# Kernel tuning notes

Measured on AMD Instinct MI355X. Metric: run time of the kernel, lower is better.

## Reference

```python
import jax, jax.numpy as jnp
import numpy as np
import math

N_HEADS = 16
EMBD = 1024
D_HEAD = EMBD // N_HEADS


def setup_inputs() -> dict:
    key = jax.random.key(0)
    ks = jax.random.split(key, 5)
    s = 1.0 / math.sqrt(EMBD)
    return {
        "x": jax.random.normal(ks[0], (2, 2048, EMBD), dtype=jnp.float32),
        "w_in": jax.random.normal(ks[1], (EMBD, 3 * EMBD), dtype=jnp.float32) * s,
        "b_in": jax.random.normal(ks[2], (3 * EMBD,), dtype=jnp.float32) * 0.02,
        "w_out": jax.random.normal(ks[3], (EMBD, EMBD), dtype=jnp.float32) * s,
        "b_out": jax.random.normal(ks[4], (EMBD,), dtype=jnp.float32) * 0.02,
    }


def reference(x, w_in, b_in, w_out, b_out):
    # x: [B, S, D]
    B, S, D = x.shape
    qkv = x @ w_in + b_in                      # [B, S, 3D]
    q, k, v = jnp.split(qkv, 3, axis=-1)
    # [B, S, H, dh] -> [B, H, S, dh]
    def heads(t):
        return t.reshape(B, S, N_HEADS, D_HEAD).transpose(0, 2, 1, 3)
    q, k, v = heads(q), heads(k), heads(v)
    scores = jnp.einsum("bhqd,bhkd->bhqk", q, k)  # [B, H, S, S]
    # causal mask applied before scaling (as in original; -inf invariant to scale)
    causal = jnp.tril(jnp.ones((S, S), dtype=bool))
    scores = jnp.where(causal, scores, -jnp.inf)
    scores = scores / jnp.asarray(math.sqrt(D_HEAD), dtype=scores.dtype)
    attn = jax.nn.softmax(scores, axis=-1)
    out = jnp.einsum("bhqk,bhkd->bhqd", attn, v)  # [B, H, S, dh]
    out = out.transpose(0, 2, 1, 3).reshape(B, S, D)
    return out @ w_out + b_out
```

## Files before the change

kernel.cpp:

```cpp
#include <hip/hip_runtime.h>
#include <stdint.h>

#define DEVI __device__ __forceinline__

typedef __attribute__((ext_vector_type(8))) short short8;
typedef __attribute__((ext_vector_type(4))) float f32x4;
typedef __attribute__((ext_vector_type(4))) uint32_t u32x4;

DEVI unsigned short f2bf(float f) {
    union { float f; uint32_t u; } v; v.f = f;
    return (unsigned short)((v.u + 0x7FFFu + ((v.u >> 16) & 1u)) >> 16);
}

DEVI uint32_t cvtpk_bf16(float a, float b) {
    uint32_t r;
    asm("v_cvt_pk_bf16_f32 %0, %1, %2" : "=v"(r) : "v"(a), "v"(b));
    return r;
}

DEVI void perm32(uint32_t &a, uint32_t &b) {
    asm("v_permlane32_swap_b32 %0, %1" : "+v"(a), "+v"(b));
}
DEVI void perm16(uint32_t &a, uint32_t &b) {
    asm("v_permlane16_swap_b32 %0, %1" : "+v"(a), "+v"(b));
}

DEVI void gload16(const void* g, void* l) {
    __builtin_amdgcn_global_load_lds(
        (const __attribute__((address_space(1))) unsigned int*)g,
        (__attribute__((address_space(3))) unsigned int*)l, 16, 0, 0);
}

__global__ void k_cvt(const float* __restrict__ in, ushort* __restrict__ out, int n4) {
    int i = blockIdx.x * blockDim.x + threadIdx.x;
    int stride = gridDim.x * blockDim.x;
    for (; i < n4; i += stride) {
        float4 v = ((const float4*)in)[i];
        ushort4 o;
        o.x = f2bf(v.x); o.y = f2bf(v.y); o.z = f2bf(v.z); o.w = f2bf(v.w);
        ((ushort4*)out)[i] = o;
    }
}

__global__ void k_tcvt(const float* __restrict__ in, ushort* __restrict__ out, int R, int C) {
    __shared__ float t[32][33];
    int c0 = blockIdx.x * 32, r0 = blockIdx.y * 32;
    int lr = threadIdx.x >> 5, lc = threadIdx.x & 31;
    #pragma unroll
    for (int i = 0; i < 4; i++)
        t[lr + 8*i][lc] = in[(size_t)(r0 + lr + 8*i)*C + c0 + lc];
    __syncthreads();
    #pragma unroll
    for (int i = 0; i < 4; i++)
        out[(size_t)(c0 + lr + 8*i)*R + r0 + lc] = f2bf(t[lc][lr + 8*i]);
}

template<int MODE, int NJ>
__global__ __launch_bounds__(256, 2) void k_gemm(
    const ushort* __restrict__ A, const ushort* __restrict__ Bt,
    const float* __restrict__ bias,
    ushort* __restrict__ oQ, ushort* __restrict__ oK, ushort* __restrict__ oV,
    float* __restrict__ oF,
    int M, int N, int K, int S)
{
    __shared__ __align__(16) ushort As[128*64];
    __shared__ __align__(16) ushort Bs[NJ*32*64];
    const int tid = threadIdx.x;
    const int w = tid >> 6, l = tid & 63;

    int lin = blockIdx.y * gridDim.x + blockIdx.x;
    int nwg = gridDim.x * gridDim.y;
    int swz = (lin & 7) * (nwg >> 3) + (lin >> 3);
    const int m0 = (swz / gridDim.x) * 128, n0 = (swz % gridDim.x) * (NJ*32);

    const int wr = (w >> 1) * 64, wc = (w & 1) * (NJ*16);
    const int fr = l & 15, fg = l >> 4;
    const int lr8 = l >> 3;
    const int slot = (l & 7) ^ lr8;

    f32x4 acc[4][NJ] = {};

    const ushort* Abase = A + (size_t)(m0 + w*32 + lr8) * K + slot*8;
    const ushort* Bbase = Bt + (size_t)(n0 + w*(NJ*8) + lr8) * K + slot*8;

    for (int k0 = 0; k0 < K; k0 += 64) {
        __syncthreads();
        #pragma unroll
        for (int i = 0; i < 4; i++)
            gload16(Abase + (size_t)(8*i)*K + k0, &As[(w*32 + 8*i)*64]);
        #pragma unroll
        for (int i = 0; i < NJ; i++)
            gload16(Bbase + (size_t)(8*i)*K + k0, &Bs[(w*(NJ*8) + 8*i)*64]);
        __syncthreads();
        #pragma unroll
        for (int kk = 0; kk < 2; kk++) {
            short8 af[4], bfr[NJ];
            #pragma unroll
            for (int i = 0; i < 4; i++) {
                int ra = wr + i*16 + fr;
                af[i] = *(const short8*)((const char*)As + ra*128 + ((kk*64 + fg*16) ^ ((ra & 7) << 4)));
            }
            #pragma unroll
            for (int j = 0; j < NJ; j++) {
                int rb = wc + j*16 + fr;
                bfr[j] = *(const short8*)((const char*)Bs + rb*128 + ((kk*64 + fg*16) ^ ((rb & 7) << 4)));
            }
            #pragma unroll
            for (int i = 0; i < 4; i++)
                #pragma unroll
                for (int j = 0; j < NJ; j++)
                    acc[i][j] = __builtin_amdgcn_mfma_f32_16x16x32_bf16(af[i], bfr[j], acc[i][j], 0, 0, 0);
        }
    }

    if (MODE == 1) {
        #pragma unroll
        for (int j = 0; j < NJ; j++) {
            int n = n0 + wc + j*16 + fr;
            float bv = bias[n];
            #pragma unroll
            for (int i = 0; i < 4; i++) {
                int mrow = m0 + wr + i*16 + fg*4;
                #pragma unroll
                for (int r = 0; r < 4; r++)
                    oF[(size_t)(mrow + r)*N + n] = acc[i][j][r] + bv;
            }
        }
    } else {
        #pragma unroll
        for (int j = 0; j < NJ; j++) {
            int n = n0 + wc + j*16 + fr;
            int region = n >> 10;
            int h = (n & 1023) >> 6;
            int d = n & 63;
            float bv = bias[n];
            float scl = (region == 0) ? 0.18033688011112042f : 1.0f;
            #pragma unroll
            for (int i = 0; i < 4; i++) {
                int mrow = m0 + wr + i*16 + fg*4;
                int b = mrow >> 11;
                int s = mrow & 2047;
                if (region < 2) {
                    ushort* dst = (region == 0 ? oQ : oK) + ((size_t)(b*16 + h)*S)*64 + (size_t)d;
                    #pragma unroll
                    for (int r = 0; r < 4; r++)
                        dst[(size_t)(s + r)*64] = f2bf((acc[i][j][r] + bv) * scl);
                } else {
                    ushort* dst = oV + ((size_t)(b*16 + h)*64 + d)*S + s;
                    ushort4 pk;
                    pk.x = f2bf(acc[i][j][0] + bv);
                    pk.y = f2bf(acc[i][j][1] + bv);
                    pk.z = f2bf(acc[i][j][2] + bv);
                    pk.w = f2bf(acc[i][j][3] + bv);
                    *(ushort4*)dst = pk;
                }
            }
        }
    }
}

__global__ __launch_bounds__(128, 2) void k_attn(
    const ushort* __restrict__ Q,
    const ushort* __restrict__ Kb,
    const ushort* __restrict__ Vt,
    ushort* __restrict__ O,
    int S)
{
    __shared__ __align__(16) ushort Kt[2][64*64];
    __shared__ __align__(16) ushort Vs[2][64*64];

    const int tid = threadIdx.x, w = tid >> 6, l = tid & 63;
    const int bid = blockIdx.x;
    const int half = bid >> 9;
    const int r_ = bid & 511;
    const int h = r_ & 15, b = (r_ >> 4) & 1, p = r_ >> 5;
    const int qt = half ? p : (31 - p);
    const int bh = b * 16 + h;
    const int qw = qt * 64 + w * 32;
    const int fr = l & 15, fg = l >> 4;

    short8 qf[2][2];
    {
        const ushort* qp = Q + ((size_t)bh*S + qw + fr)*64 + fg*8;
        qf[0][0] = *(const short8*)(qp);
        qf[0][1] = *(const short8*)(qp + 32);
        qf[1][0] = *(const short8*)(qp + 16*64);
        qf[1][1] = *(const short8*)(qp + 16*64 + 32);
    }

    float l_[2] = {0.f, 0.f};
    f32x4 o_[2][4] = {};

    const int lr8 = l >> 3;
    const int slot = (l & 7) ^ lr8;
    const ushort* Ksrc = Kb + (size_t)bh*S*64;
    const ushort* Vsrc = Vt + (size_t)bh*64*S;

    const int nt = qt + 1;

    auto stage = [&](int buf, int j0) {
        #pragma unroll
        for (int i = 0; i < 4; i++) {
            int rb = w*32 + i*8;
            gload16(Ksrc + (size_t)(j0 + rb + lr8)*64 + slot*8, &Kt[buf][rb*64]);
            gload16(Vsrc + (size_t)(rb + lr8)*S + j0 + slot*8, &Vs[buf][rb*64]);
        }
    };

    stage(0, 0);
    __syncthreads();
    int cur = 0;

    for (int jt = 0; jt < nt; jt++) {
        const int j0 = jt * 64;
        if (jt + 1 < nt) stage(cur ^ 1, j0 + 64);

        f32x4 sa[2][4] = {};
        __builtin_amdgcn_s_setprio(1);
        #pragma unroll
        for (int kk = 0; kk < 2; kk++) {
            short8 kf[4];
            #pragma unroll
            for (int f = 0; f < 4; f++) {
                int row = f*16 + fr;
                kf[f] = *(const short8*)((const char*)Kt[cur] + row*128 + ((kk*64 + fg*16) ^ ((row & 7) << 4)));
            }
            #pragma unroll
            for (int t = 0; t < 2; t++)
                #pragma unroll
                for (int f = 0; f < 4; f++)
                    sa[t][f] = __builtin_amdgcn_mfma_f32_16x16x32_bf16(kf[f], qf[t][kk], sa[t][f], 0, 0, 0);
        }
        __builtin_amdgcn_s_setprio(0);

        if (jt == nt - 1) {
            #pragma unroll
            for (int t = 0; t < 2; t++) {
                int qg = qw + t*16 + fr;
                #pragma unroll
                for (int f = 0; f < 4; f++) {
                    int base = j0 + f*16 + fg*4 - qg;
                    #pragma unroll
                    for (int r = 0; r < 4; r++)
                        if (base + r > 0) sa[t][f][r] = -1e30f;
                }
            }
        }

        uint32_t cw[2][4][2];
        #pragma unroll
        for (int t = 0; t < 2; t++)
            #pragma unroll
            for (int f = 0; f < 4; f++) {
                float p0 = __builtin_amdgcn_exp2f(sa[t][f][0]);
                float p1 = __builtin_amdgcn_exp2f(sa[t][f][1]);
                float p2 = __builtin_amdgcn_exp2f(sa[t][f][2]);
                float p3 = __builtin_amdgcn_exp2f(sa[t][f][3]);
                l_[t] += (p0 + p1) + (p2 + p3);
                cw[t][f][0] = cvtpk_bf16(p0, p1);
                cw[t][f][1] = cvtpk_bf16(p2, p3);
            }

        __builtin_amdgcn_s_setprio(1);
        #pragma unroll
        for (int kk = 0; kk < 2; kk++) {
            short8 pf[2];
            #pragma unroll
            for (int t = 0; t < 2; t++) {
                uint32_t a0 = cw[t][2*kk][0], b0 = cw[t][2*kk + 1][0];
                perm32(a0, b0); perm16(a0, b0);
                uint32_t a1 = cw[t][2*kk][1], b1 = cw[t][2*kk + 1][1];
                perm32(a1, b1); perm16(a1, b1);
                u32x4 uw; uw[0] = a0; uw[1] = a1; uw[2] = b0; uw[3] = b1;
                pf[t] = __builtin_bit_cast(short8, uw);
            }
            #pragma unroll
            for (int f = 0; f < 4; f++) {
                int row = f*16 + fr;
                short8 vf = *(const short8*)((const char*)Vs[cur] + row*128 + ((kk*64 + fg*16) ^ ((row & 7) << 4)));
                #pragma unroll
                for (int t = 0; t < 2; t++)
                    o_[t][f] = __builtin_amdgcn_mfma_f32_16x16x32_bf16(vf, pf[t], o_[t][f], 0, 0, 0);
            }
        }
        __builtin_amdgcn_s_setprio(0);

        __syncthreads();
        cur ^= 1;
    }

    #pragma unroll
    for (int t = 0; t < 2; t++) {
        l_[t] += __shfl_xor(l_[t], 16);
        l_[t] += __shfl_xor(l_[t], 32);
    }

    #pragma unroll
    for (int t = 0; t < 2; t++) {
        float inv = 1.0f / l_[t];
        int qg = qw + t*16 + fr;
        #pragma unroll
        for (int f = 0; f < 4; f++) {
            ushort4 pk;
            pk.x = f2bf(o_[t][f][0] * inv);
            pk.y = f2bf(o_[t][f][1] * inv);
            pk.z = f2bf(o_[t][f][2] * inv);
            pk.w = f2bf(o_[t][f][3] * inv);
            *(ushort4*)&O[((size_t)(b*S + qg))*1024 + h*64 + f*16 + fg*4] = pk;
        }
    }
}

extern "C" void kernel_launch(void* const* d_in, const int* in_sizes, int n_in,
                              void* d_out, int out_size, void* d_ws, size_t ws_size,
                              hipStream_t stream)
{
    const float* x     = (const float*)d_in[0];
    const float* w_in  = (const float*)d_in[1];
    const float* b_in  = (const float*)d_in[2];
    const float* w_out = (const float*)d_in[3];
    const float* b_out = (const float*)d_in[4];
    float* out = (float*)d_out;

    const int B = 2, S = 2048, D = 1024, H = 16;
    const int M = B * S;

    if (ws_size < (40u << 20)) return;
    char* ws = (char*)d_ws;
    ushort* xb     = (ushort*)(ws);
    ushort* w_inT  = (ushort*)(ws + (8u << 20));
    ushort* w_outT = (ushort*)(ws + (14u << 20));
    ushort* qb     = (ushort*)(ws + (16u << 20));
    ushort* kb     = (ushort*)(ws + (24u << 20));
    ushort* vtb    = (ushort*)(ws + (32u << 20));

    k_cvt<<<2048, 256, 0, stream>>>(x, xb, M*D/4);
    k_tcvt<<<dim3(3*D/32, D/32), 256, 0, stream>>>(w_in, w_inT, D, 3*D);
    k_tcvt<<<dim3(D/32, D/32), 256, 0, stream>>>(w_out, w_outT, D, D);
    k_gemm<0,4><<<dim3(3*D/128, M/128), 256, 0, stream>>>(xb, w_inT, b_in, qb, kb, vtb, nullptr, M, 3*D, D, S);
    k_attn<<<1024, 128, 0, stream>>>(qb, kb, vtb, xb, S);
    k_gemm<1,2><<<dim3(D/64, M/128), 256, 0, stream>>>(xb, w_outT, b_out, nullptr, nullptr, nullptr, out, M, D, D, S);
}
```

Before: 108.0 us.

## Split long causal query tiles across two KV chunks and add combine kernel

The longer query tiles (qt 16-31) are now processed by two blocks, each covering half of the KV range. The shorter tiles stay as single blocks, which raises the attention grid from 1024 to 1536 blocks. Each split block writes its unnormalized bf16 partial output and row sums to workspace, and a new k_comb kernel adds the halves and normalizes them. The goal is to even out the causal workload and shorten the tail of long blocks. In exchange it adds a kernel launch, extra global traffic for the partials, and some bf16 rounding of the unnormalized partial sums.

Measured after the change: 109.5 us. No clear change (+1.4%).

```diff
diff --git a/kernel.cpp b/kernel.cpp
--- a/kernel.cpp
+++ b/kernel.cpp
@@ -10,6 +10,11 @@
 DEVI unsigned short f2bf(float f) {
     union { float f; uint32_t u; } v; v.f = f;
     return (unsigned short)((v.u + 0x7FFFu + ((v.u >> 16) & 1u)) >> 16);
+}
+
+DEVI float bf2f(unsigned short u) {
+    union { uint32_t u; float f; } v; v.u = ((uint32_t)u) << 16;
+    return v.f;
 }
 
 DEVI uint32_t cvtpk_bf16(float a, float b) {
@@ -164,6 +169,8 @@
     const ushort* __restrict__ Kb,
     const ushort* __restrict__ Vt,
     ushort* __restrict__ O,
+    ushort* __restrict__ po,
+    float* __restrict__ pl,
     int S)
 {
     __shared__ __align__(16) ushort Kt[2][64*64];
@@ -171,13 +178,24 @@
 
     const int tid = threadIdx.x, w = tid >> 6, l = tid & 63;
     const int bid = blockIdx.x;
-    const int half = bid >> 9;
-    const int r_ = bid & 511;
-    const int h = r_ & 15, b = (r_ >> 4) & 1, p = r_ >> 5;
-    const int qt = half ? p : (31 - p);
-    const int bh = b * 16 + h;
+    int qt, c, bh;
+    if (bid < 1024) {
+        bh = bid & 31;
+        c = (bid >> 5) & 1;
+        qt = 31 - (bid >> 6);
+    } else {
+        int r = bid - 1024;
+        bh = r & 31;
+        c = -1;
+        qt = 15 - (r >> 5);
+    }
+    const int b = bh >> 4, h = bh & 15;
     const int qw = qt * 64 + w * 32;
     const int fr = l & 15, fg = l >> 4;
+
+    const int len0 = (qt + 2) >> 1;
+    const int t0 = (c == 1) ? len0 : 0;
+    const int t1 = (c == 0) ? len0 : qt + 1;
 
     short8 qf[2][2];
     {
@@ -196,8 +214,6 @@
     const ushort* Ksrc = Kb + (size_t)bh*S*64;
     const ushort* Vsrc = Vt + (size_t)bh*64*S;
 
-    const int nt = qt + 1;
-
     auto stage = [&](int buf, int j0) {
         #pragma unroll
         for (int i = 0; i < 4; i++) {
@@ -207,13 +223,13 @@
         }
     };
 
-    stage(0, 0);
+    stage(0, t0 * 64);
     __syncthreads();
     int cur = 0;
 
-    for (int jt = 0; jt < nt; jt++) {
+    for (int jt = t0; jt < t1; jt++) {
         const int j0 = jt * 64;
-        if (jt + 1 < nt) stage(cur ^ 1, j0 + 64);
+        if (jt + 1 < t1) stage(cur ^ 1, j0 + 64);
 
         f32x4 sa[2][4] = {};
         __builtin_amdgcn_s_setprio(1);
@@ -233,7 +249,7 @@
         }
         __builtin_amdgcn_s_setprio(0);
 
-        if (jt == nt - 1) {
+        if (jt == qt) {
             #pragma unroll
             for (int t = 0; t < 2; t++) {
                 int qg = qw + t*16 + fr;
@@ -295,19 +311,68 @@
         l_[t] += __shfl_xor(l_[t], 32);
     }
 
+    if (c < 0) {
+        #pragma unroll
+        for (int t = 0; t < 2; t++) {
+            float inv = 1.0f / l_[t];
+            int qg = qw + t*16 + fr;
+            #pragma unroll
+            for (int f = 0; f < 4; f++) {
+                ushort4 pk;
+                pk.x = f2bf(o_[t][f][0] * inv);
+                pk.y = f2bf(o_[t][f][1] * inv);
+                pk.z = f2bf(o_[t][f][2] * inv);
+                pk.w = f2bf(o_[t][f][3] * inv);
+                *(ushort4*)&O[((size_t)(b*S + qg))*1024 + h*64 + f*16 + fg*4] = pk;
+            }
+        }
+    } else {
+        const int idx = (((31 - qt) << 1) | c) * 32 + bh;
+        ushort* pob = po + ((size_t)idx * 2 + w) * 2048;
+        #pragma unroll
+        for (int t = 0; t < 2; t++) {
+            #pragma unroll
+            for (int f = 0; f < 4; f++) {
+                uint2 pk;
+                pk.x = cvtpk_bf16(o_[t][f][0], o_[t][f][1]);
+                pk.y = cvtpk_bf16(o_[t][f][2], o_[t][f][3]);
+                *(uint2*)(pob + (t*4 + f)*256 + fr*16 + fg*4) = pk;
+            }
+            if (fg == 0) pl[(size_t)idx*64 + w*32 + t*16 + fr] = l_[t];
+        }
+    }
+}
+
+__global__ __launch_bounds__(256) void k_comb(
+    const ushort* __restrict__ po, const float* __restrict__ pl,
+    ushort* __restrict__ O, int S)
+{
+    const int bx = blockIdx.x;
+    const int qt = 31 - (bx >> 5);
+    const int bh = bx & 31;
+    const int b = bh >> 4, h = bh & 15;
+    const int iA = ((31 - qt) << 1) * 32 + bh;
+    const int iB = iA + 32;
+    const float* la = pl + (size_t)iA * 64;
+    const float* lb = pl + (size_t)iB * 64;
+
     #pragma unroll
-    for (int t = 0; t < 2; t++) {
-        float inv = 1.0f / l_[t];
-        int qg = qw + t*16 + fr;
-        #pragma unroll
-        for (int f = 0; f < 4; f++) {
-            ushort4 pk;
-            pk.x = f2bf(o_[t][f][0] * inv);
-            pk.y = f2bf(o_[t][f][1] * inv);
-            pk.z = f2bf(o_[t][f][2] * inv);
-            pk.w = f2bf(o_[t][f][3] * inv);
-            *(ushort4*)&O[((size_t)(b*S + qg))*1024 + h*64 + f*16 + fg*4] = pk;
-        }
+    for (int k = 0; k < 4; k++) {
+        int ss = threadIdx.x + 256 * k;
+        int w = (ss >> 9) & 1, t = (ss >> 8) & 1, f = (ss >> 6) & 3, fr = (ss >> 2) & 15, fg = ss & 3;
+        int g = ss & 511;
+        int row = w*32 + t*16 + fr;
+        ushort4 va = *(const ushort4*)(po + ((size_t)iA * 2 + w) * 2048 + g * 4);
+        ushort4 vb = *(const ushort4*)(po + ((size_t)iB * 2 + w) * 2048 + g * 4);
+        float den = la[row] + lb[row];
+        float inv = 1.0f / fmaxf(den, 1e-30f);
+        ushort4 pk;
+        pk.x = f2bf((bf2f(va.x) + bf2f(vb.x)) * inv);
+        pk.y = f2bf((bf2f(va.y) + bf2f(vb.y)) * inv);
+        pk.z = f2bf((bf2f(va.z) + bf2f(vb.z)) * inv);
+        pk.w = f2bf((bf2f(va.w) + bf2f(vb.w)) * inv);
+        int q = qt*64 + row;
+        *(ushort4*)&O[((size_t)(b*S + q))*1024 + h*64 + f*16 + fg*4] = pk;
     }
 }
 
@@ -325,7 +390,7 @@
     const int B = 2, S = 2048, D = 1024, H = 16;
     const int M = B * S;
 
-    if (ws_size < (40u << 20)) return;
+    if (ws_size < (52u << 20)) return;
     char* ws = (char*)d_ws;
     ushort* xb     = (ushort*)(ws);
     ushort* w_inT  = (ushort*)(ws + (8u << 20));
@@ -333,11 +398,14 @@
     ushort* qb     = (ushort*)(ws + (16u << 20));
     ushort* kb     = (ushort*)(ws + (24u << 20));
     ushort* vtb    = (ushort*)(ws + (32u << 20));
+    ushort* po     = (ushort*)(ws + (40u << 20));
+    float*  pl     = (float*)(ws + (48u << 20));
 
     k_cvt<<<2048, 256, 0, stream>>>(x, xb, M*D/4);
     k_tcvt<<<dim3(3*D/32, D/32), 256, 0, stream>>>(w_in, w_inT, D, 3*D);
     k_tcvt<<<dim3(D/32, D/32), 256, 0, stream>>>(w_out, w_outT, D, D);
     k_gemm<0,4><<<dim3(3*D/128, M/128), 256, 0, stream>>>(xb, w_inT, b_in, qb, kb, vtb, nullptr, M, 3*D, D, S);
-    k_attn<<<1024, 128, 0, stream>>>(qb, kb, vtb, xb, S);
+    k_attn<<<1536, 128, 0, stream>>>(qb, kb, vtb, xb, po, pl, S);
+    k_comb<<<512, 256, 0, stream>>>(po, pl, xb, S);
     k_gemm<1,2><<<dim3(D/64, M/128), 256, 0, stream>>>(xb, w_outT, b_out, nullptr, nullptr, nullptr, out, M, D, D, S);
 }
```
